# Optimization experiments

Hardware: AMD Instinct MI355X
Metric: run time of the kernel (lower is better)

The kernel has to match this reference:

```python
import jax, jax.numpy as jnp
import numpy as np

WINDOW = 10  # hard-coded window_size in the source module
B, D, K, V = 16384, 1024, 64, 64


def _tri():
    # lower triangle = +1e5, strict upper triangle = -1e5, shape (1, W, W)
    t = (np.tril(np.full((WINDOW, WINDOW), 2.0, dtype='float32')) - 1) * 100000.0
    return jnp.asarray(t.reshape(1, WINDOW, WINDOW))


def setup_inputs() -> dict:
    key = jax.random.key(0)
    kx, kk, kq, kv = jax.random.split(key, 4)
    return {
        "x": jax.random.normal(kx, (B, WINDOW, D), dtype=jnp.float32),
        "wk": jax.random.uniform(kk, (D, K), dtype=jnp.float32),
        "wq": jax.random.uniform(kq, (D, K), dtype=jnp.float32),
        "wv": jax.random.uniform(kv, (D, V), dtype=jnp.float32),
    }


def reference(x, wk, wq, wv):
    # projections: (B, W, D) @ (D, K/V)
    k = x @ wk
    q = x @ wq
    v = x @ wv
    # NOTE: source computes k @ q^T (row index = key position), no 1/sqrt(d) scaling
    scores = jnp.einsum('bik,bjk->bij', k, q)  # (B, W, W)
    # causal-style mask via elementwise MINIMUM with +/-1e5 triangular matrix
    masked = jnp.minimum(scores, _tri())
    a = jax.nn.softmax(masked, axis=2)
    return a @ v  # (B, W, V)
```

## Files before the change

kernel.cpp:

```cpp
#include <hip/hip_runtime.h>


#define D 1024
#define BM 80
#define KCHUNKS 16
#define ASTR 72
#define APIECE 11520
#define ABUF 23040
#define KQSTR 133
#define VSTR 65
#define SCOFF 42560
#define SMEMSZ 46080
#define SCL 4.8828125e-4f

typedef __attribute__((ext_vector_type(8))) _Float16 f16x8;
typedef __attribute__((ext_vector_type(4))) float f32x4;
typedef __attribute__((ext_vector_type(4))) unsigned short u16x4;

__global__ __launch_bounds__(256) void prep_w(const float* __restrict__ wk,
                                              const float* __restrict__ wq,
                                              const float* __restrict__ wv,
                                              unsigned short* __restrict__ wth,
                                              unsigned short* __restrict__ wtl) {
    int idx = blockIdx.x * 256 + threadIdx.x;
    int n  = idx >> 10;
    int kk = idx & 1023;
    const float* src = (n < 64) ? wk : (n < 128) ? wq : wv;
    float w = src[kk * 64 + (n & 63)];
    _Float16 h = (_Float16)w;
    float r = (w - (float)h) * 2048.0f;
    _Float16 l = (_Float16)r;
    wth[idx] = __builtin_bit_cast(unsigned short, h);
    wtl[idx] = __builtin_bit_cast(unsigned short, l);
}

__global__ __launch_bounds__(256, 3) void fused_attn(
        const float* __restrict__ x,
        const unsigned short* __restrict__ wth,
        const unsigned short* __restrict__ wtl,
        float* __restrict__ out) {

    __shared__ char smem[SMEMSZ];
    float* kq  = (float*)smem;
    float* vv  = (float*)smem;
    float* scw = (float*)(smem + SCOFF);

    const int tid  = threadIdx.x;
    const int wave = tid >> 6;
    const int lane = tid & 63;
    const int m0   = blockIdx.x * BM;
    const int nbase = wave * 48;
    const int arow  = lane & 15;
    const int apart = lane >> 4;

    f16x8 aprobe = {}, bone = {}, aone = {}, bcol = {};
    if (apart == 0) {
        aprobe[0] = (_Float16)(float)(arow + 1);
        bone[0]   = (_Float16)1.0f;
        aone[0]   = (_Float16)1.0f;
        bcol[0]   = (_Float16)(float)(arow + 1);
    }
    f32x4 z = {0.f, 0.f, 0.f, 0.f};
    f32x4 d1 = __builtin_amdgcn_mfma_f32_16x16x32_f16(aprobe, bone, z, 0, 0, 0);
    f32x4 d2 = __builtin_amdgcn_mfma_f32_16x16x32_f16(aone,  bcol, z, 0, 0, 0);
    int R[4], Cc[4];
    #pragma unroll
    for (int r = 0; r < 4; ++r) {
        R[r]  = (int)(d1[r] + 0.5f) - 1;
        Cc[r] = (int)(d2[r] + 0.5f) - 1;
    }

    int srow[5], scol[5];
    #pragma unroll
    for (int it = 0; it < 5; ++it) {
        int p = tid + it * 256;
        srow[it] = p >> 4;
        scol[it] = (p & 15) << 2;
    }

    f32x4 acc[5][3] = {};

    {
        float4 xv[5];
        #pragma unroll
        for (int it = 0; it < 5; ++it)
            xv[it] = *reinterpret_cast<const float4*>(
                x + (size_t)(m0 + srow[it]) * D + scol[it]);
        unsigned short* H = (unsigned short*)smem;
        unsigned short* L = (unsigned short*)(smem + APIECE);
        #pragma unroll
        for (int it = 0; it < 5; ++it) {
            u16x4 hh, ll;
            #pragma unroll
            for (int e = 0; e < 4; ++e) {
                float xe = (e == 0) ? xv[it].x : (e == 1) ? xv[it].y : (e == 2) ? xv[it].z : xv[it].w;
                _Float16 h = (_Float16)xe;
                float rl = (xe - (float)h) * 2048.0f;
                _Float16 l = (_Float16)rl;
                hh[e] = __builtin_bit_cast(unsigned short, h);
                ll[e] = __builtin_bit_cast(unsigned short, l);
            }
            int ro = srow[it] * ASTR + scol[it];
            *reinterpret_cast<u16x4*>(H + ro) = hh;
            *reinterpret_cast<u16x4*>(L + ro) = ll;
        }
    }
    __syncthreads();

    for (int t = 0; t < KCHUNKS; ++t) {
        char* curb = smem + (t & 1) * ABUF;
        char* nxtb = smem + ((t + 1) & 1) * ABUF;

        float4 xv[5];
        if (t < KCHUNKS - 1) {
            #pragma unroll
            for (int it = 0; it < 5; ++it)
                xv[it] = *reinterpret_cast<const float4*>(
                    x + (size_t)(m0 + srow[it]) * D + (t + 1) * 64 + scol[it]);
        }

        #pragma unroll
        for (int ks = 0; ks < 2; ++ks) {
            f16x8 wfh[3], wfl[3];
            #pragma unroll
            for (int nt = 0; nt < 3; ++nt) {
                int n = nbase + nt * 16 + arow;
                size_t off = (size_t)n * D + t * 64 + ks * 32 + apart * 8;
                wfh[nt] = *reinterpret_cast<const f16x8*>(wth + off);
                wfl[nt] = *reinterpret_cast<const f16x8*>(wtl + off);
            }
            #pragma unroll
            for (int mt = 0; mt < 5; ++mt) {
                int ab = (mt * 16 + arow) * (ASTR * 2) + (ks * 4 + apart) * 16;
                f16x8 ah = *reinterpret_cast<const f16x8*>(curb + ab);
                f16x8 al = *reinterpret_cast<const f16x8*>(curb + APIECE + ab);
                #pragma unroll
                for (int nt = 0; nt < 3; ++nt) {
                    acc[mt][nt] = __builtin_amdgcn_mfma_f32_16x16x32_f16(ah, wfh[nt], acc[mt][nt], 0, 0, 0);
                    f32x4 tt = {0.f, 0.f, 0.f, 0.f};
                    tt = __builtin_amdgcn_mfma_f32_16x16x32_f16(ah, wfl[nt], tt, 0, 0, 0);
                    tt = __builtin_amdgcn_mfma_f32_16x16x32_f16(al, wfh[nt], tt, 0, 0, 0);
                    #pragma unroll
                    for (int c = 0; c < 4; ++c)
                        acc[mt][nt][c] = fmaf(tt[c], SCL, acc[mt][nt][c]);
                }
            }
        }

        if (t < KCHUNKS - 1) {
            unsigned short* H = (unsigned short*)nxtb;
            unsigned short* L = (unsigned short*)(nxtb + APIECE);
            #pragma unroll
            for (int it = 0; it < 5; ++it) {
                u16x4 hh, ll;
                #pragma unroll
                for (int e = 0; e < 4; ++e) {
                    float xe = (e == 0) ? xv[it].x : (e == 1) ? xv[it].y : (e == 2) ? xv[it].z : xv[it].w;
                    _Float16 h = (_Float16)xe;
                    float rl = (xe - (float)h) * 2048.0f;
                    _Float16 l = (_Float16)rl;
                    hh[e] = __builtin_bit_cast(unsigned short, h);
                    ll[e] = __builtin_bit_cast(unsigned short, l);
                }
                int ro = srow[it] * ASTR + scol[it];
                *reinterpret_cast<u16x4*>(H + ro) = hh;
                *reinterpret_cast<u16x4*>(L + ro) = ll;
            }
        }
        __syncthreads();
    }

    #pragma unroll
    for (int mt = 0; mt < 5; ++mt) {
        #pragma unroll
        for (int r = 0; r < 4; ++r) {
            int row = mt * 16 + R[r];
            #pragma unroll
            for (int nt = 0; nt < 3; ++nt) {
                int colbase = nbase + nt * 16;
                if (colbase < 128)
                    kq[row * KQSTR + colbase + Cc[r]] = acc[mt][nt][r];
            }
        }
    }
    __syncthreads();

    float* sc0 = scw + wave * 220;
    #pragma unroll
    for (int bb = 0; bb < 2; ++bb) {
        const int r0 = (wave * 2 + bb) * 10;
        float* sc = sc0 + bb * 110;
        #pragma unroll
        for (int it = 0; it < 2; ++it) {
            int p = it * 64 + lane;
            if (p < 100) {
                int i = p / 10;
                int j = p - i * 10;
                double s = 0.0;
                #pragma unroll 8
                for (int c = 0; c < 64; ++c)
                    s += (double)kq[(r0 + i) * KQSTR + c] *
                         (double)kq[(r0 + j) * KQSTR + 64 + c];
                double lim = (j <= i) ? 1e5 : -1e5;
                sc[i * 11 + j] = (float)fmin(s, lim);
            }
        }
    }
    __syncthreads();

    if (lane < 10) {
        int i = lane;
        #pragma unroll
        for (int bb = 0; bb < 2; ++bb) {
            float* sc = sc0 + bb * 110;
            double vals[10];
            double mx = -1e300;
            #pragma unroll
            for (int j = 0; j < 10; ++j) { vals[j] = (double)sc[i * 11 + j]; mx = fmax(mx, vals[j]); }
            double sum = 0.0;
            #pragma unroll
            for (int j = 0; j < 10; ++j) { vals[j] = exp(vals[j] - mx); sum += vals[j]; }
            double inv = 1.0 / sum;
            #pragma unroll
            for (int j = 0; j < 10; ++j) sc[i * 11 + j] = (float)(vals[j] * inv);
        }
    }
    #pragma unroll
    for (int mt = 0; mt < 5; ++mt) {
        #pragma unroll
        for (int r = 0; r < 4; ++r) {
            int row = mt * 16 + R[r];
            #pragma unroll
            for (int nt = 0; nt < 3; ++nt) {
                int colbase = nbase + nt * 16;
                if (colbase >= 128)
                    vv[row * VSTR + (colbase - 128) + Cc[r]] = acc[mt][nt][r];
            }
        }
    }
    __syncthreads();

    #pragma unroll
    for (int bb = 0; bb < 2; ++bb) {
        const int bloc = wave * 2 + bb;
        const int r0   = bloc * 10;
        float* sc = sc0 + bb * 110;
        size_t ob = (size_t)(blockIdx.x * 8 + bloc) * 640;
        #pragma unroll
        for (int i = 0; i < 10; ++i) {
            double o = 0.0;
            #pragma unroll
            for (int j = 0; j < 10; ++j)
                o += (double)sc[i * 11 + j] * (double)vv[(r0 + j) * VSTR + lane];
            out[ob + (size_t)i * 64 + lane] = (float)o;
        }
    }
}

extern "C" void kernel_launch(void* const* d_in, const int* in_sizes, int n_in,
                              void* d_out, int out_size, void* d_ws, size_t ws_size,
                              hipStream_t stream) {
    const float* x  = (const float*)d_in[0];
    const float* wk = (const float*)d_in[1];
    const float* wq = (const float*)d_in[2];
    const float* wv = (const float*)d_in[3];
    unsigned short* wth = (unsigned short*)d_ws;
    unsigned short* wtl = wth + 192 * 1024;
    float* outp = (float*)d_out;

    prep_w<<<768, 256, 0, stream>>>(wk, wq, wv, wth, wtl);
    fused_attn<<<2048, 256, 0, stream>>>(x, wth, wtl, outp);
}
```

Before: 307.9 us.

## Warp-specialize: one producer wave stages x, three waves run MFMA

Splits the block into a dedicated producer wave, which loads and converts the next x chunk into the split-f16 LDS buffers, and three consumer waves that each compute 64 output columns with MFMA. Previously all four waves both loaded and computed 48 columns each. The goal is to overlap global loads and conversion with matrix math without each wave carrying prefetch registers. In exchange, only three of four waves issue MFMAs, each consumer holds more accumulators, and one wave must now stream the whole 80x64 chunk by itself, which could become the bottleneck.

```diff
diff --git a/kernel.cpp b/kernel.cpp
--- a/kernel.cpp
+++ b/kernel.cpp
@@ -34,6 +34,55 @@
     wtl[idx] = __builtin_bit_cast(unsigned short, l);
 }
 
+static __device__ __forceinline__ void stage_chunk(
+        const float* __restrict__ x, char* buf, int m0, int t, int lane) {
+    unsigned short* H = (unsigned short*)buf;
+    unsigned short* L = (unsigned short*)(buf + APIECE);
+    const float* xc = x + (size_t)m0 * D + t * 64;
+    float4 xa[5], xb[5];
+    #pragma unroll
+    for (int it = 0; it < 5; ++it) {
+        int p = lane + it * 64;
+        xa[it] = *reinterpret_cast<const float4*>(
+            xc + (size_t)(p >> 4) * D + ((p & 15) << 2));
+    }
+    #pragma unroll
+    for (int b = 0; b < 4; ++b) {
+        if (b < 3) {
+            #pragma unroll
+            for (int it = 0; it < 5; ++it) {
+                int p = lane + (b * 5 + 5 + it) * 64;
+                xb[it] = *reinterpret_cast<const float4*>(
+                    xc + (size_t)(p >> 4) * D + ((p & 15) << 2));
+            }
+        }
+        #pragma unroll
+        for (int it = 0; it < 5; ++it) {
+            int p = lane + (b * 5 + it) * 64;
+            int row = p >> 4;
+            int c4  = (p & 15) << 2;
+            float4 xv = xa[it];
+            u16x4 hh, ll;
+            #pragma unroll
+            for (int e = 0; e < 4; ++e) {
+                float xe = (e == 0) ? xv.x : (e == 1) ? xv.y : (e == 2) ? xv.z : xv.w;
+                _Float16 h = (_Float16)xe;
+                float rl = (xe - (float)h) * 2048.0f;
+                _Float16 l = (_Float16)rl;
+                hh[e] = __builtin_bit_cast(unsigned short, h);
+                ll[e] = __builtin_bit_cast(unsigned short, l);
+            }
+            int ro = row * ASTR + c4;
+            *reinterpret_cast<u16x4*>(H + ro) = hh;
+            *reinterpret_cast<u16x4*>(L + ro) = ll;
+        }
+        if (b < 3) {
+            #pragma unroll
+            for (int it = 0; it < 5; ++it) xa[it] = xb[it];
+        }
+    }
+}
+
 __global__ __launch_bounds__(256, 3) void fused_attn(
         const float* __restrict__ x,
         const unsigned short* __restrict__ wth,
@@ -49,9 +98,9 @@
     const int wave = tid >> 6;
     const int lane = tid & 63;
     const int m0   = blockIdx.x * BM;
-    const int nbase = wave * 48;
     const int arow  = lane & 15;
     const int apart = lane >> 4;
+    const int nbase = wave * 64;
 
     f16x8 aprobe = {}, bone = {}, aone = {}, bcol = {};
     if (apart == 0) {
@@ -70,116 +119,60 @@
         Cc[r] = (int)(d2[r] + 0.5f) - 1;
     }
 
-    int srow[5], scol[5];
-    #pragma unroll
-    for (int it = 0; it < 5; ++it) {
-        int p = tid + it * 256;
-        srow[it] = p >> 4;
-        scol[it] = (p & 15) << 2;
-    }
-
-    f32x4 acc[5][3] = {};
-
-    {
-        float4 xv[5];
-        #pragma unroll
-        for (int it = 0; it < 5; ++it)
-            xv[it] = *reinterpret_cast<const float4*>(
-                x + (size_t)(m0 + srow[it]) * D + scol[it]);
-        unsigned short* H = (unsigned short*)smem;
-        unsigned short* L = (unsigned short*)(smem + APIECE);
-        #pragma unroll
-        for (int it = 0; it < 5; ++it) {
-            u16x4 hh, ll;
-            #pragma unroll
-            for (int e = 0; e < 4; ++e) {
-                float xe = (e == 0) ? xv[it].x : (e == 1) ? xv[it].y : (e == 2) ? xv[it].z : xv[it].w;
-                _Float16 h = (_Float16)xe;
-                float rl = (xe - (float)h) * 2048.0f;
-                _Float16 l = (_Float16)rl;
-                hh[e] = __builtin_bit_cast(unsigned short, h);
-                ll[e] = __builtin_bit_cast(unsigned short, l);
-            }
-            int ro = srow[it] * ASTR + scol[it];
-            *reinterpret_cast<u16x4*>(H + ro) = hh;
-            *reinterpret_cast<u16x4*>(L + ro) = ll;
-        }
-    }
+    f32x4 acc[5][4] = {};
+
+    if (wave == 3) stage_chunk(x, smem, m0, 0, lane);
     __syncthreads();
 
     for (int t = 0; t < KCHUNKS; ++t) {
-        char* curb = smem + (t & 1) * ABUF;
-        char* nxtb = smem + ((t + 1) & 1) * ABUF;
-
-        float4 xv[5];
-        if (t < KCHUNKS - 1) {
-            #pragma unroll
-            for (int it = 0; it < 5; ++it)
-                xv[it] = *reinterpret_cast<const float4*>(
-                    x + (size_t)(m0 + srow[it]) * D + (t + 1) * 64 + scol[it]);
-        }
-
-        #pragma unroll
-        for (int ks = 0; ks < 2; ++ks) {
-            f16x8 wfh[3], wfl[3];
-            #pragma unroll
-            for (int nt = 0; nt < 3; ++nt) {
-                int n = nbase + nt * 16 + arow;
-                size_t off = (size_t)n * D + t * 64 + ks * 32 + apart * 8;
-                wfh[nt] = *reinterpret_cast<const f16x8*>(wth + off);
-                wfl[nt] = *reinterpret_cast<const f16x8*>(wtl + off);
-            }
-            #pragma unroll
-            for (int mt = 0; mt < 5; ++mt) {
-                int ab = (mt * 16 + arow) * (ASTR * 2) + (ks * 4 + apart) * 16;
-                f16x8 ah = *reinterpret_cast<const f16x8*>(curb + ab);
-                f16x8 al = *reinterpret_cast<const f16x8*>(curb + APIECE + ab);
-                #pragma unroll
-                for (int nt = 0; nt < 3; ++nt) {
-                    acc[mt][nt] = __builtin_amdgcn_mfma_f32_16x16x32_f16(ah, wfh[nt], acc[mt][nt], 0, 0, 0);
-                    f32x4 tt = {0.f, 0.f, 0.f, 0.f};
-                    tt = __builtin_amdgcn_mfma_f32_16x16x32_f16(ah, wfl[nt], tt, 0, 0, 0);
-                    tt = __builtin_amdgcn_mfma_f32_16x16x32_f16(al, wfh[nt], tt, 0, 0, 0);
+        if (wave < 3) {
+            char* curb = smem + (t & 1) * ABUF;
+            #pragma unroll
+            for (int ks = 0; ks < 2; ++ks) {
+                f16x8 wfh[4], wfl[4];
+                #pragma unroll
+                for (int nt = 0; nt < 4; ++nt) {
+                    int n = nbase + nt * 16 + arow;
+                    size_t off = (size_t)n * D + t * 64 + ks * 32 + apart * 8;
+                    wfh[nt] = *reinterpret_cast<const f16x8*>(wth + off);
+                    wfl[nt] = *reinterpret_cast<const f16x8*>(wtl + off);
+                }
+                #pragma unroll
+                for (int mt = 0; mt < 5; ++mt) {
+                    int ab = (mt * 16 + arow) * (ASTR * 2) + (ks * 4 + apart) * 16;
+                    f16x8 ah = *reinterpret_cast<const f16x8*>(curb + ab);
+                    f16x8 al = *reinterpret_cast<const f16x8*>(curb + APIECE + ab);
                     #pragma unroll
-                    for (int c = 0; c < 4; ++c)
-                        acc[mt][nt][c] = fmaf(tt[c], SCL, acc[mt][nt][c]);
-                }
-            }
-        }
-
-        if (t < KCHUNKS - 1) {
-            unsigned short* H = (unsigned short*)nxtb;
-            unsigned short* L = (unsigned short*)(nxtb + APIECE);
-            #pragma unroll
-            for (int it = 0; it < 5; ++it) {
-                u16x4 hh, ll;
-                #pragma unroll
-                for (int e = 0; e < 4; ++e) {
-                    float xe = (e == 0) ? xv[it].x : (e == 1) ? xv[it].y : (e == 2) ? xv[it].z : xv[it].w;
-                    _Float16 h = (_Float16)xe;
-                    float rl = (xe - (float)h) * 2048.0f;
-                    _Float16 l = (_Float16)rl;
-                    hh[e] = __builtin_bit_cast(unsigned short, h);
-                    ll[e] = __builtin_bit_cast(unsigned short, l);
-                }
-                int ro = srow[it] * ASTR + scol[it];
-                *reinterpret_cast<u16x4*>(H + ro) = hh;
-                *reinterpret_cast<u16x4*>(L + ro) = ll;
-            }
+                    for (int nt = 0; nt < 4; ++nt) {
+                        acc[mt][nt] = __builtin_amdgcn_mfma_f32_16x16x32_f16(ah, wfh[nt], acc[mt][nt], 0, 0, 0);
+                        f32x4 tt = {0.f, 0.f, 0.f, 0.f};
+                        tt = __builtin_amdgcn_mfma_f32_16x16x32_f16(ah, wfl[nt], tt, 0, 0, 0);
+                        tt = __builtin_amdgcn_mfma_f32_16x16x32_f16(al, wfh[nt], tt, 0, 0, 0);
+                        #pragma unroll
+                        for (int c = 0; c < 4; ++c)
+                            acc[mt][nt][c] = fmaf(tt[c], SCL, acc[mt][nt][c]);
+                    }
+                }
+            }
+        } else {
+            if (t < KCHUNKS - 1)
+                stage_chunk(x, smem + ((t + 1) & 1) * ABUF, m0, t + 1, lane);
         }
         __syncthreads();
     }
 
-    #pragma unroll
-    for (int mt = 0; mt < 5; ++mt) {
-        #pragma unroll
-        for (int r = 0; r < 4; ++r) {
-            int row = mt * 16 + R[r];
-            #pragma unroll
-            for (int nt = 0; nt < 3; ++nt) {
-                int colbase = nbase + nt * 16;
-                if (colbase < 128)
-                    kq[row * KQSTR + colbase + Cc[r]] = acc[mt][nt][r];
+    if (wave < 3) {
+        #pragma unroll
+        for (int mt = 0; mt < 5; ++mt) {
+            #pragma unroll
+            for (int r = 0; r < 4; ++r) {
+                int row = mt * 16 + R[r];
+                #pragma unroll
+                for (int nt = 0; nt < 4; ++nt) {
+                    int colbase = nbase + nt * 16;
+                    if (colbase < 128)
+                        kq[row * KQSTR + colbase + Cc[r]] = acc[mt][nt][r];
+                }
             }
         }
     }
@@ -225,16 +218,18 @@
             for (int j = 0; j < 10; ++j) sc[i * 11 + j] = (float)(vals[j] * inv);
         }
     }
-    #pragma unroll
-    for (int mt = 0; mt < 5; ++mt) {
-        #pragma unroll
-        for (int r = 0; r < 4; ++r) {
-            int row = mt * 16 + R[r];
-            #pragma unroll
-            for (int nt = 0; nt < 3; ++nt) {
-                int colbase = nbase + nt * 16;
-                if (colbase >= 128)
-                    vv[row * VSTR + (colbase - 128) + Cc[r]] = acc[mt][nt][r];
+    if (wave < 3) {
+        #pragma unroll
+        for (int mt = 0; mt < 5; ++mt) {
+            #pragma unroll
+            for (int r = 0; r < 4; ++r) {
+                int row = mt * 16 + R[r];
+                #pragma unroll
+                for (int nt = 0; nt < 4; ++nt) {
+                    int colbase = nbase + nt * 16;
+                    if (colbase >= 128)
+                        vv[row * VSTR + (colbase - 128) + Cc[r]] = acc[mt][nt][r];
+                }
             }
         }
     }
```

Result: slower. 765.2 us (+148.6%).

## Split block into producer and consumer waves for x staging and MFMA

Applied to the files above, without the earlier changes.

Doubles the block to 512 threads: waves 0-3 run the MFMA projection with raised scheduling priority, while waves 4-7 load the next x chunk, split it into fp16 hi/lo pieces and write it to LDS. The epilogue gives each of the 8 waves one batch element instead of two. The goal is to overlap global loads and conversion with the matrix math without raising per-wave register pressure. The cost is more threads per block, fewer resident blocks per CU, and idle producer waves during the epilogue.

```diff
diff --git a/kernel.cpp b/kernel.cpp
--- a/kernel.cpp
+++ b/kernel.cpp
@@ -34,7 +34,7 @@
     wtl[idx] = __builtin_bit_cast(unsigned short, l);
 }
 
-__global__ __launch_bounds__(256, 3) void fused_attn(
+__global__ __launch_bounds__(512, 4) void fused_attn(
         const float* __restrict__ x,
         const unsigned short* __restrict__ wth,
         const unsigned short* __restrict__ wtl,
@@ -49,9 +49,10 @@
     const int wave = tid >> 6;
     const int lane = tid & 63;
     const int m0   = blockIdx.x * BM;
-    const int nbase = wave * 48;
     const int arow  = lane & 15;
     const int apart = lane >> 4;
+    const bool consumer = (wave < 4);
+    const int nbase = wave * 48;
 
     f16x8 aprobe = {}, bone = {}, aone = {}, bcol = {};
     if (apart == 0) {
@@ -71,23 +72,26 @@
     }
 
     int srow[5], scol[5];
-    #pragma unroll
-    for (int it = 0; it < 5; ++it) {
-        int p = tid + it * 256;
-        srow[it] = p >> 4;
-        scol[it] = (p & 15) << 2;
+    {
+        int s = ((wave & 3) << 6) | lane;
+        #pragma unroll
+        for (int it = 0; it < 5; ++it) {
+            int p = s + it * 256;
+            srow[it] = p >> 4;
+            scol[it] = (p & 15) << 2;
+        }
     }
 
     f32x4 acc[5][3] = {};
 
-    {
+    if (!consumer) {
+        unsigned short* H = (unsigned short*)smem;
+        unsigned short* L = (unsigned short*)(smem + APIECE);
         float4 xv[5];
         #pragma unroll
         for (int it = 0; it < 5; ++it)
             xv[it] = *reinterpret_cast<const float4*>(
                 x + (size_t)(m0 + srow[it]) * D + scol[it]);
-        unsigned short* H = (unsigned short*)smem;
-        unsigned short* L = (unsigned short*)(smem + APIECE);
         #pragma unroll
         for (int it = 0; it < 5; ++it) {
             u16x4 hh, ll;
@@ -108,48 +112,46 @@
     __syncthreads();
 
     for (int t = 0; t < KCHUNKS; ++t) {
-        char* curb = smem + (t & 1) * ABUF;
-        char* nxtb = smem + ((t + 1) & 1) * ABUF;
-
-        float4 xv[5];
-        if (t < KCHUNKS - 1) {
+        if (consumer) {
+            char* curb = smem + (t & 1) * ABUF;
+            __builtin_amdgcn_s_setprio(1);
+            #pragma unroll
+            for (int ks = 0; ks < 2; ++ks) {
+                f16x8 wfh[3], wfl[3];
+                #pragma unroll
+                for (int nt = 0; nt < 3; ++nt) {
+                    int n = nbase + nt * 16 + arow;
+                    size_t off = (size_t)n * D + t * 64 + ks * 32 + apart * 8;
+                    wfh[nt] = *reinterpret_cast<const f16x8*>(wth + off);
+                    wfl[nt] = *reinterpret_cast<const f16x8*>(wtl + off);
+                }
+                #pragma unroll
+                for (int mt = 0; mt < 5; ++mt) {
+                    int ab = (mt * 16 + arow) * (ASTR * 2) + (ks * 4 + apart) * 16;
+                    f16x8 ah = *reinterpret_cast<const f16x8*>(curb + ab);
+                    f16x8 al = *reinterpret_cast<const f16x8*>(curb + APIECE + ab);
+                    #pragma unroll
+                    for (int nt = 0; nt < 3; ++nt) {
+                        acc[mt][nt] = __builtin_amdgcn_mfma_f32_16x16x32_f16(ah, wfh[nt], acc[mt][nt], 0, 0, 0);
+                        f32x4 tt = {0.f, 0.f, 0.f, 0.f};
+                        tt = __builtin_amdgcn_mfma_f32_16x16x32_f16(ah, wfl[nt], tt, 0, 0, 0);
+                        tt = __builtin_amdgcn_mfma_f32_16x16x32_f16(al, wfh[nt], tt, 0, 0, 0);
+                        #pragma unroll
+                        for (int c = 0; c < 4; ++c)
+                            acc[mt][nt][c] = fmaf(tt[c], SCL, acc[mt][nt][c]);
+                    }
+                }
+            }
+            __builtin_amdgcn_s_setprio(0);
+        } else if (t < KCHUNKS - 1) {
+            char* nxtb = smem + ((t + 1) & 1) * ABUF;
+            unsigned short* H = (unsigned short*)nxtb;
+            unsigned short* L = (unsigned short*)(nxtb + APIECE);
+            float4 xv[5];
             #pragma unroll
             for (int it = 0; it < 5; ++it)
                 xv[it] = *reinterpret_cast<const float4*>(
                     x + (size_t)(m0 + srow[it]) * D + (t + 1) * 64 + scol[it]);
-        }
-
-        #pragma unroll
-        for (int ks = 0; ks < 2; ++ks) {
-            f16x8 wfh[3], wfl[3];
-            #pragma unroll
-            for (int nt = 0; nt < 3; ++nt) {
-                int n = nbase + nt * 16 + arow;
-                size_t off = (size_t)n * D + t * 64 + ks * 32 + apart * 8;
-                wfh[nt] = *reinterpret_cast<const f16x8*>(wth + off);
-                wfl[nt] = *reinterpret_cast<const f16x8*>(wtl + off);
-            }
-            #pragma unroll
-            for (int mt = 0; mt < 5; ++mt) {
-                int ab = (mt * 16 + arow) * (ASTR * 2) + (ks * 4 + apart) * 16;
-                f16x8 ah = *reinterpret_cast<const f16x8*>(curb + ab);
-                f16x8 al = *reinterpret_cast<const f16x8*>(curb + APIECE + ab);
-                #pragma unroll
-                for (int nt = 0; nt < 3; ++nt) {
-                    acc[mt][nt] = __builtin_amdgcn_mfma_f32_16x16x32_f16(ah, wfh[nt], acc[mt][nt], 0, 0, 0);
-                    f32x4 tt = {0.f, 0.f, 0.f, 0.f};
-                    tt = __builtin_amdgcn_mfma_f32_16x16x32_f16(ah, wfl[nt], tt, 0, 0, 0);
-                    tt = __builtin_amdgcn_mfma_f32_16x16x32_f16(al, wfh[nt], tt, 0, 0, 0);
-                    #pragma unroll
-                    for (int c = 0; c < 4; ++c)
-                        acc[mt][nt][c] = fmaf(tt[c], SCL, acc[mt][nt][c]);
-                }
-            }
-        }
-
-        if (t < KCHUNKS - 1) {
-            unsigned short* H = (unsigned short*)nxtb;
-            unsigned short* L = (unsigned short*)(nxtb + APIECE);
             #pragma unroll
             for (int it = 0; it < 5; ++it) {
                 u16x4 hh, ll;
@@ -170,82 +172,74 @@
         __syncthreads();
     }
 
+    if (consumer) {
+        #pragma unroll
+        for (int mt = 0; mt < 5; ++mt) {
+            #pragma unroll
+            for (int r = 0; r < 4; ++r) {
+                int row = mt * 16 + R[r];
+                #pragma unroll
+                for (int nt = 0; nt < 3; ++nt) {
+                    int colbase = nbase + nt * 16;
+                    if (colbase < 128)
+                        kq[row * KQSTR + colbase + Cc[r]] = acc[mt][nt][r];
+                }
+            }
+        }
+    }
+    __syncthreads();
+
+    const int r0 = wave * 10;
+    float* sc = scw + wave * 110;
     #pragma unroll
-    for (int mt = 0; mt < 5; ++mt) {
-        #pragma unroll
-        for (int r = 0; r < 4; ++r) {
-            int row = mt * 16 + R[r];
-            #pragma unroll
-            for (int nt = 0; nt < 3; ++nt) {
-                int colbase = nbase + nt * 16;
-                if (colbase < 128)
-                    kq[row * KQSTR + colbase + Cc[r]] = acc[mt][nt][r];
-            }
-        }
-    }
-    __syncthreads();
-
-    float* sc0 = scw + wave * 220;
-    #pragma unroll
-    for (int bb = 0; bb < 2; ++bb) {
-        const int r0 = (wave * 2 + bb) * 10;
-        float* sc = sc0 + bb * 110;
-        #pragma unroll
-        for (int it = 0; it < 2; ++it) {
-            int p = it * 64 + lane;
-            if (p < 100) {
-                int i = p / 10;
-                int j = p - i * 10;
-                double s = 0.0;
-                #pragma unroll 8
-                for (int c = 0; c < 64; ++c)
-                    s += (double)kq[(r0 + i) * KQSTR + c] *
-                         (double)kq[(r0 + j) * KQSTR + 64 + c];
-                double lim = (j <= i) ? 1e5 : -1e5;
-                sc[i * 11 + j] = (float)fmin(s, lim);
-            }
+    for (int it = 0; it < 2; ++it) {
+        int p = it * 64 + lane;
+        if (p < 100) {
+            int i = p / 10;
+            int j = p - i * 10;
+            double s = 0.0;
+            #pragma unroll 8
+            for (int c = 0; c < 64; ++c)
+                s += (double)kq[(r0 + i) * KQSTR + c] *
+                     (double)kq[(r0 + j) * KQSTR + 64 + c];
+            double lim = (j <= i) ? 1e5 : -1e5;
+            sc[i * 11 + j] = (float)fmin(s, lim);
         }
     }
     __syncthreads();
 
     if (lane < 10) {
         int i = lane;
-        #pragma unroll
-        for (int bb = 0; bb < 2; ++bb) {
-            float* sc = sc0 + bb * 110;
-            double vals[10];
-            double mx = -1e300;
-            #pragma unroll
-            for (int j = 0; j < 10; ++j) { vals[j] = (double)sc[i * 11 + j]; mx = fmax(mx, vals[j]); }
-            double sum = 0.0;
-            #pragma unroll
-            for (int j = 0; j < 10; ++j) { vals[j] = exp(vals[j] - mx); sum += vals[j]; }
-            double inv = 1.0 / sum;
-            #pragma unroll
-            for (int j = 0; j < 10; ++j) sc[i * 11 + j] = (float)(vals[j] * inv);
-        }
-    }
-    #pragma unroll
-    for (int mt = 0; mt < 5; ++mt) {
-        #pragma unroll
-        for (int r = 0; r < 4; ++r) {
-            int row = mt * 16 + R[r];
-            #pragma unroll
-            for (int nt = 0; nt < 3; ++nt) {
-                int colbase = nbase + nt * 16;
-                if (colbase >= 128)
-                    vv[row * VSTR + (colbase - 128) + Cc[r]] = acc[mt][nt][r];
-            }
-        }
-    }
-    __syncthreads();
-
-    #pragma unroll
-    for (int bb = 0; bb < 2; ++bb) {
-        const int bloc = wave * 2 + bb;
-        const int r0   = bloc * 10;
-        float* sc = sc0 + bb * 110;
-        size_t ob = (size_t)(blockIdx.x * 8 + bloc) * 640;
+        double vals[10];
+        double mx = -1e300;
+        #pragma unroll
+        for (int j = 0; j < 10; ++j) { vals[j] = (double)sc[i * 11 + j]; mx = fmax(mx, vals[j]); }
+        double sum = 0.0;
+        #pragma unroll
+        for (int j = 0; j < 10; ++j) { vals[j] = exp(vals[j] - mx); sum += vals[j]; }
+        double inv = 1.0 / sum;
+        #pragma unroll
+        for (int j = 0; j < 10; ++j) sc[i * 11 + j] = (float)(vals[j] * inv);
+    }
+    if (consumer) {
+        #pragma unroll
+        for (int mt = 0; mt < 5; ++mt) {
+            #pragma unroll
+            for (int r = 0; r < 4; ++r) {
+                int row = mt * 16 + R[r];
+                #pragma unroll
+                for (int nt = 0; nt < 3; ++nt) {
+                    int colbase = nbase + nt * 16;
+                    if (colbase >= 128)
+                        vv[row * VSTR + (colbase - 128) + Cc[r]] = acc[mt][nt][r];
+                }
+            }
+        }
+    }
+    __syncthreads();
+
+    {
+        size_t ob = (size_t)(blockIdx.x * 8 + wave) * 640;
         #pragma unroll
         for (int i = 0; i < 10; ++i) {
             double o = 0.0;
@@ -269,5 +263,5 @@
     float* outp = (float*)d_out;
 
     prep_w<<<768, 256, 0, stream>>>(wk, wq, wv, wth, wtl);
-    fused_attn<<<2048, 256, 0, stream>>>(x, wth, wtl, outp);
+    fused_attn<<<2048, 512, 0, stream>>>(x, wth, wtl, outp);
 }
```

New measurement: 364.7 us. 1.18x slower.

## Replace double-buffered 64-wide K chunks with single-buffered 128-wide chunks

Applied to the files above, without the earlier changes.

Drops the register-prefetched double buffer for the split fp16 x tile and uses one 128-column buffer per K step, halving the number of chunks and barriers. Global loads of x are no longer overlapped with the MFMA work on the previous chunk; each step loads, converts, syncs, then computes. This trades latency hiding for fewer syncs and lower register pressure.

```diff
diff --git a/kernel.cpp b/kernel.cpp
--- a/kernel.cpp
+++ b/kernel.cpp
@@ -3,10 +3,10 @@
 
 #define D 1024
 #define BM 80
-#define KCHUNKS 16
-#define ASTR 72
-#define APIECE 11520
-#define ABUF 23040
+#define KCHUNKS 8
+#define BK 128
+#define ASTR 136
+#define APIECE 21760
 #define KQSTR 133
 #define VSTR 65
 #define SCOFF 42560
@@ -41,6 +41,8 @@
         float* __restrict__ out) {
 
     __shared__ char smem[SMEMSZ];
+    unsigned short* AhS = (unsigned short*)smem;
+    unsigned short* AlS = (unsigned short*)(smem + APIECE);
     float* kq  = (float*)smem;
     float* vv  = (float*)smem;
     float* scw = (float*)(smem + SCOFF);
@@ -70,70 +72,58 @@
         Cc[r] = (int)(d2[r] + 0.5f) - 1;
     }
 
-    int srow[5], scol[5];
-    #pragma unroll
-    for (int it = 0; it < 5; ++it) {
-        int p = tid + it * 256;
-        srow[it] = p >> 4;
-        scol[it] = (p & 15) << 2;
-    }
-
     f32x4 acc[5][3] = {};
 
-    {
-        float4 xv[5];
-        #pragma unroll
-        for (int it = 0; it < 5; ++it)
-            xv[it] = *reinterpret_cast<const float4*>(
-                x + (size_t)(m0 + srow[it]) * D + scol[it]);
-        unsigned short* H = (unsigned short*)smem;
-        unsigned short* L = (unsigned short*)(smem + APIECE);
-        #pragma unroll
-        for (int it = 0; it < 5; ++it) {
-            u16x4 hh, ll;
-            #pragma unroll
-            for (int e = 0; e < 4; ++e) {
-                float xe = (e == 0) ? xv[it].x : (e == 1) ? xv[it].y : (e == 2) ? xv[it].z : xv[it].w;
-                _Float16 h = (_Float16)xe;
-                float rl = (xe - (float)h) * 2048.0f;
-                _Float16 l = (_Float16)rl;
-                hh[e] = __builtin_bit_cast(unsigned short, h);
-                ll[e] = __builtin_bit_cast(unsigned short, l);
-            }
-            int ro = srow[it] * ASTR + scol[it];
-            *reinterpret_cast<u16x4*>(H + ro) = hh;
-            *reinterpret_cast<u16x4*>(L + ro) = ll;
-        }
-    }
-    __syncthreads();
-
     for (int t = 0; t < KCHUNKS; ++t) {
-        char* curb = smem + (t & 1) * ABUF;
-        char* nxtb = smem + ((t + 1) & 1) * ABUF;
-
-        float4 xv[5];
-        if (t < KCHUNKS - 1) {
-            #pragma unroll
-            for (int it = 0; it < 5; ++it)
+        __syncthreads();
+        #pragma unroll
+        for (int b = 0; b < 2; ++b) {
+            float4 xv[5];
+            #pragma unroll
+            for (int it = 0; it < 5; ++it) {
+                int p   = tid + (b * 5 + it) * 256;
+                int row = p >> 5;
+                int c4  = (p & 31) << 2;
                 xv[it] = *reinterpret_cast<const float4*>(
-                    x + (size_t)(m0 + srow[it]) * D + (t + 1) * 64 + scol[it]);
-        }
-
-        #pragma unroll
-        for (int ks = 0; ks < 2; ++ks) {
+                    x + (size_t)(m0 + row) * D + t * BK + c4);
+            }
+            #pragma unroll
+            for (int it = 0; it < 5; ++it) {
+                int p   = tid + (b * 5 + it) * 256;
+                int row = p >> 5;
+                int c4  = (p & 31) << 2;
+                u16x4 hh, ll;
+                #pragma unroll
+                for (int e = 0; e < 4; ++e) {
+                    float xe = (e == 0) ? xv[it].x : (e == 1) ? xv[it].y : (e == 2) ? xv[it].z : xv[it].w;
+                    _Float16 h = (_Float16)xe;
+                    float rl = (xe - (float)h) * 2048.0f;
+                    _Float16 l = (_Float16)rl;
+                    hh[e] = __builtin_bit_cast(unsigned short, h);
+                    ll[e] = __builtin_bit_cast(unsigned short, l);
+                }
+                int ro = row * ASTR + c4;
+                *reinterpret_cast<u16x4*>(AhS + ro) = hh;
+                *reinterpret_cast<u16x4*>(AlS + ro) = ll;
+            }
+        }
+        __syncthreads();
+
+        #pragma unroll
+        for (int ks = 0; ks < 4; ++ks) {
             f16x8 wfh[3], wfl[3];
             #pragma unroll
             for (int nt = 0; nt < 3; ++nt) {
                 int n = nbase + nt * 16 + arow;
-                size_t off = (size_t)n * D + t * 64 + ks * 32 + apart * 8;
+                size_t off = (size_t)n * D + t * BK + ks * 32 + apart * 8;
                 wfh[nt] = *reinterpret_cast<const f16x8*>(wth + off);
                 wfl[nt] = *reinterpret_cast<const f16x8*>(wtl + off);
             }
             #pragma unroll
             for (int mt = 0; mt < 5; ++mt) {
                 int ab = (mt * 16 + arow) * (ASTR * 2) + (ks * 4 + apart) * 16;
-                f16x8 ah = *reinterpret_cast<const f16x8*>(curb + ab);
-                f16x8 al = *reinterpret_cast<const f16x8*>(curb + APIECE + ab);
+                f16x8 ah = *reinterpret_cast<const f16x8*>((char*)AhS + ab);
+                f16x8 al = *reinterpret_cast<const f16x8*>((char*)AlS + ab);
                 #pragma unroll
                 for (int nt = 0; nt < 3; ++nt) {
                     acc[mt][nt] = __builtin_amdgcn_mfma_f32_16x16x32_f16(ah, wfh[nt], acc[mt][nt], 0, 0, 0);
@@ -146,29 +136,8 @@
                 }
             }
         }
-
-        if (t < KCHUNKS - 1) {
-            unsigned short* H = (unsigned short*)nxtb;
-            unsigned short* L = (unsigned short*)(nxtb + APIECE);
-            #pragma unroll
-            for (int it = 0; it < 5; ++it) {
-                u16x4 hh, ll;
-                #pragma unroll
-                for (int e = 0; e < 4; ++e) {
-                    float xe = (e == 0) ? xv[it].x : (e == 1) ? xv[it].y : (e == 2) ? xv[it].z : xv[it].w;
-                    _Float16 h = (_Float16)xe;
-                    float rl = (xe - (float)h) * 2048.0f;
-                    _Float16 l = (_Float16)rl;
-                    hh[e] = __builtin_bit_cast(unsigned short, h);
-                    ll[e] = __builtin_bit_cast(unsigned short, l);
-                }
-                int ro = srow[it] * ASTR + scol[it];
-                *reinterpret_cast<u16x4*>(H + ro) = hh;
-                *reinterpret_cast<u16x4*>(L + ro) = ll;
-            }
-        }
-        __syncthreads();
-    }
+    }
+    __syncthreads();
 
     #pragma unroll
     for (int mt = 0; mt < 5; ++mt) {
```

Measured after the change: 382.3 us. 24.2% more time.
